# Optimization experiments

Measured on AMD Instinct MI355X. Metric: run time of the kernel, lower is better.

## Reference

```python
import jax, jax.numpy as jnp
import numpy as np

NH = 4
ATT = 16
COL = 64
AIS = 64
B = 8192
SK = 200


def setup_inputs() -> dict:
    key = jax.random.key(0)
    k1, k2, k3, k4, k5 = jax.random.split(key, 5)
    # Xavier-uniform bounds for [fan_in, fan_out] matrices
    def xavier(k, fan_in, fan_out):
        bound = float(np.sqrt(6.0 / (fan_in + fan_out)))
        return jax.random.uniform(k, (fan_in, fan_out), jnp.float32, -bound, bound)
    return {
        "query_input": jax.random.normal(k1, (B, 1, COL), jnp.float32),
        "action_list_input": jax.random.normal(k2, (B, SK, AIS), jnp.float32),
        "Q": xavier(k3, COL, ATT * NH),
        "K": xavier(k4, AIS, ATT * NH),
        "V": xavier(k5, AIS, ATT * NH),
    }


def reference(query_input, action_list_input, Q, K, V):
    b = query_input.shape[0]
    sq = query_input.shape[1]          # == 1 (required by final reshape)
    sk = action_list_input.shape[1]
    # projections
    q = jnp.tensordot(query_input, Q, axes=([-1], [0]))        # [B,Sq,NH*ATT]
    k = jnp.tensordot(action_list_input, K, axes=([-1], [0]))  # [B,Sk,NH*ATT]
    v = jnp.tensordot(action_list_input, V, axes=([-1], [0]))  # [B,Sk,NH*ATT]
    # split heads: chunk along last dim then stack on new leading dim -> [NH,B,S,ATT]
    qh = jnp.transpose(q.reshape(b, sq, NH, ATT), (2, 0, 1, 3))
    kh = jnp.transpose(k.reshape(b, sk, NH, ATT), (2, 0, 1, 3))
    vh = jnp.transpose(v.reshape(b, sk, NH, ATT), (2, 0, 1, 3))
    scores = jnp.einsum("hbqd,hbkd->hbqk", qh, kh) / 8.0       # [NH,B,Sq,Sk]
    attn = jax.nn.softmax(scores, axis=-1)
    res = jnp.einsum("hbqk,hbkd->hbqd", attn, vh)              # [NH,B,Sq,ATT]
    res = jnp.transpose(res, (1, 2, 0, 3))                     # [B,Sq,NH,ATT]
    return res.reshape(b, NH * ATT)
```

## Files before the change

kernel.cpp:

```cpp
#include <hip/hip_runtime.h>

#define NH   4
#define ATT  16
#define COL  64
#define AIS  64
#define SK   200
#define HD   64
#define JP   32
#define AROW 33

typedef _Float16 half2v __attribute__((ext_vector_type(2)));
typedef unsigned int uint32;

static __device__ __forceinline__ half2v u2h(uint32 u) {
    union { uint32 u; half2v h; } x; x.u = u; return x.h;
}

static __device__ __forceinline__ uint32 pk_u32(float a, float b) {
#if __has_builtin(__builtin_amdgcn_cvt_pkrtz)
    union { decltype(__builtin_amdgcn_cvt_pkrtz(0.f, 0.f)) h; uint32 u; } x;
    x.h = __builtin_amdgcn_cvt_pkrtz(a, b);
    return x.u;
#else
    union { half2v h; uint32 u; } x;
    x.h.x = (_Float16)a; x.h.y = (_Float16)b;
    return x.u;
#endif
}

#if __has_builtin(__builtin_amdgcn_fdot2)
#define DOT2(a, b, c) __builtin_amdgcn_fdot2((a), (b), (c), false)
#else
#define DOT2(a, b, c) fmaf((float)(a).x, (float)(b).x, fmaf((float)(a).y, (float)(b).y, (c)))
#endif

__global__ __launch_bounds__(256, 4)
void fused_attn_kernel(const float* __restrict__ query,
                       const float* __restrict__ action,
                       const float* __restrict__ Qw,
                       const float* __restrict__ Kw,
                       const float* __restrict__ Vw,
                       float* __restrict__ out) {
    __shared__ uint32 A2[SK * AROW];
    __shared__ float4 p4_s[SK];
    __shared__ float4 wpart[4][64];
    __shared__ float4 w4_s[64];
    __shared__ float  invd_s[NH];
    __shared__ float  qh_s[HD];
    __shared__ __align__(16) uint32 qk4_s[JP * 4];

    const int b    = blockIdx.x;
    const int t    = threadIdx.x;
    const int lane = t & 63;
    const int wv   = t >> 6;

    const float4* act4 = (const float4*)(action + (size_t)b * (SK * AIS));
    float4 sv[13];
    #pragma unroll
    for (int i = 0; i < 12; ++i) sv[i] = act4[i * 256 + t];
    if (t < 128) sv[12] = act4[3072 + t];

    const float* qb = query + (size_t)b * COL;
    if (t < HD) {
        float acc = 0.f;
        #pragma unroll
        for (int c = 0; c < COL; ++c)
            acc = fmaf(qb[c], Qw[c * HD + t], acc);
        qh_s[t] = acc;
    }
    __syncthreads();

    if (t < 128) {
        const int h = t >> 5, jp = t & 31;
        float a0 = 0.f, a1 = 0.f;
        #pragma unroll
        for (int d = 0; d < ATT; ++d) {
            const float q = qh_s[h * ATT + d];
            a0 = fmaf(q, Kw[(2 * jp)     * HD + h * ATT + d], a0);
            a1 = fmaf(q, Kw[(2 * jp + 1) * HD + h * ATT + d], a1);
        }
        qk4_s[jp * 4 + h] = pk_u32(a0 * 0.125f, a1 * 0.125f);
    }

    #pragma unroll
    for (int i = 0; i < 12; ++i) {
        const int idx = i * 256 + t;
        const float4 v = sv[i];
        const int k   = idx >> 4;
        const int jp0 = (idx & 15) * 2;
        A2[k * AROW + jp0]     = pk_u32(v.x, v.y);
        A2[k * AROW + jp0 + 1] = pk_u32(v.z, v.w);
    }
    if (t < 128) {
        const int idx = 3072 + t;
        const float4 v = sv[12];
        const int k   = idx >> 4;
        const int jp0 = (idx & 15) * 2;
        A2[k * AROW + jp0]     = pk_u32(v.x, v.y);
        A2[k * AROW + jp0 + 1] = pk_u32(v.z, v.w);
    }
    __syncthreads();

    if (t < SK) {
        float a0 = 0.f, a1 = 0.f, a2 = 0.f, a3 = 0.f;
        const int base = t * AROW;
        const uint4* qk4 = (const uint4*)qk4_s;
        #pragma unroll 8
        for (int jp = 0; jp < JP; ++jp) {
            const half2v av = u2h(A2[base + jp]);
            const uint4 q4 = qk4[jp];
            a0 = DOT2(av, u2h(q4.x), a0);
            a1 = DOT2(av, u2h(q4.y), a1);
            a2 = DOT2(av, u2h(q4.z), a2);
            a3 = DOT2(av, u2h(q4.w), a3);
        }
        float4 s; s.x = a0; s.y = a1; s.z = a2; s.w = a3;
        p4_s[t] = s;
    }
    __syncthreads();

    {
        float* pf = (float*)p4_s;
        const int h = wv;
        const float s0 = pf[lane * 4 + h];
        const float s1 = pf[(lane + 64) * 4 + h];
        const float s2 = pf[(lane + 128) * 4 + h];
        const float s3 = (lane < SK - 192) ? pf[(lane + 192) * 4 + h] : -1e30f;
        float m = fmaxf(fmaxf(s0, s1), fmaxf(s2, s3));
        #pragma unroll
        for (int off = 32; off; off >>= 1) m = fmaxf(m, __shfl_xor(m, off));
        const float e0 = __expf(s0 - m);
        const float e1 = __expf(s1 - m);
        const float e2 = __expf(s2 - m);
        const float e3 = (lane < SK - 192) ? __expf(s3 - m) : 0.f;
        pf[lane * 4 + h]         = e0;
        pf[(lane + 64) * 4 + h]  = e1;
        pf[(lane + 128) * 4 + h] = e2;
        if (lane < SK - 192) pf[(lane + 192) * 4 + h] = e3;
        float sum = e0 + e1 + e2 + e3;
        #pragma unroll
        for (int off = 32; off; off >>= 1) sum += __shfl_xor(sum, off);
        if (lane == 0) invd_s[h] = 1.f / sum;
    }
    __syncthreads();

    {
        const int j  = lane;
        const int jp = j >> 1;
        const int k0 = wv * 50;
        float c0 = 0.f, c1 = 0.f, c2 = 0.f, c3 = 0.f;
        #pragma unroll 10
        for (int kk = 0; kk < 50; ++kk) {
            const int k = k0 + kk;
            const float4 p = p4_s[k];
            const half2v av = u2h(A2[k * AROW + jp]);
            const float a = (j & 1) ? (float)av.y : (float)av.x;
            c0 = fmaf(p.x, a, c0);
            c1 = fmaf(p.y, a, c1);
            c2 = fmaf(p.z, a, c2);
            c3 = fmaf(p.w, a, c3);
        }
        float4 c; c.x = c0; c.y = c1; c.z = c2; c.w = c3;
        wpart[wv][j] = c;
    }
    __syncthreads();

    if (t < 64) {
        const float4 r0 = wpart[0][t], r1 = wpart[1][t];
        const float4 r2 = wpart[2][t], r3 = wpart[3][t];
        float4 w;
        w.x = (r0.x + r1.x + r2.x + r3.x) * invd_s[0];
        w.y = (r0.y + r1.y + r2.y + r3.y) * invd_s[1];
        w.z = (r0.z + r1.z + r2.z + r3.z) * invd_s[2];
        w.w = (r0.w + r1.w + r2.w + r3.w) * invd_s[3];
        w4_s[t] = w;
    }
    __syncthreads();

    if (t < 64) {
        const int h = t >> 4;
        const float* wf = (const float*)w4_s;
        float acc = 0.f;
        #pragma unroll
        for (int j = 0; j < AIS; ++j)
            acc = fmaf(wf[j * 4 + h], Vw[j * HD + t], acc);
        out[(size_t)b * HD + t] = acc;
    }
}

extern "C" void kernel_launch(void* const* d_in, const int* in_sizes, int n_in,
                              void* d_out, int out_size, void* d_ws, size_t ws_size,
                              hipStream_t stream) {
    const float* query  = (const float*)d_in[0];
    const float* action = (const float*)d_in[1];
    const float* Qw     = (const float*)d_in[2];
    const float* Kw     = (const float*)d_in[3];
    const float* Vw     = (const float*)d_in[4];
    float* outp = (float*)d_out;

    (void)d_ws; (void)ws_size;

    const int B = in_sizes[0] / COL;
    fused_attn_kernel<<<B, 256, 0, stream>>>(query, action, Qw, Kw, Vw, outp);
}
```

Baseline: 545.3 us.

## Make blocks persistent over 16 batches with double-buffered LDS prefetch

Each workgroup now processes 16 consecutive batch rows instead of one. While the current batch is being computed, it loads the next batch's action tile into registers, then converts and stores it into a second LDS buffer. The Q projection and the q·K products for all 16 batches are computed once up front. This is meant to hide global-load latency behind compute and to spread the setup cost over many rows. The trade-off is a grid of only B/16 workgroups, double the LDS footprint and launch bounds of 2, which lowers occupancy and puts more weight on the in-block barriers.

```diff
diff --git a/kernel.cpp b/kernel.cpp
--- a/kernel.cpp
+++ b/kernel.cpp
@@ -8,6 +8,7 @@
 #define HD   64
 #define JP   32
 #define AROW 33
+#define NBPB 16
 
 typedef _Float16 half2v __attribute__((ext_vector_type(2)));
 typedef unsigned int uint32;
@@ -34,157 +35,202 @@
 #define DOT2(a, b, c) fmaf((float)(a).x, (float)(b).x, fmaf((float)(a).y, (float)(b).y, (c)))
 #endif
 
-__global__ __launch_bounds__(256, 4)
-void fused_attn_kernel(const float* __restrict__ query,
-                       const float* __restrict__ action,
-                       const float* __restrict__ Qw,
-                       const float* __restrict__ Kw,
-                       const float* __restrict__ Vw,
-                       float* __restrict__ out) {
-    __shared__ uint32 A2[SK * AROW];
-    __shared__ float4 p4_s[SK];
-    __shared__ float4 wpart[4][64];
-    __shared__ float4 w4_s[64];
-    __shared__ float  invd_s[NH];
-    __shared__ float  qh_s[HD];
-    __shared__ __align__(16) uint32 qk4_s[JP * 4];
-
-    const int b    = blockIdx.x;
-    const int t    = threadIdx.x;
-    const int lane = t & 63;
-    const int wv   = t >> 6;
-
-    const float4* act4 = (const float4*)(action + (size_t)b * (SK * AIS));
-    float4 sv[13];
-    #pragma unroll
-    for (int i = 0; i < 12; ++i) sv[i] = act4[i * 256 + t];
-    if (t < 128) sv[12] = act4[3072 + t];
-
-    const float* qb = query + (size_t)b * COL;
-    if (t < HD) {
-        float acc = 0.f;
-        #pragma unroll
-        for (int c = 0; c < COL; ++c)
-            acc = fmaf(qb[c], Qw[c * HD + t], acc);
-        qh_s[t] = acc;
-    }
-    __syncthreads();
-
-    if (t < 128) {
-        const int h = t >> 5, jp = t & 31;
-        float a0 = 0.f, a1 = 0.f;
-        #pragma unroll
-        for (int d = 0; d < ATT; ++d) {
-            const float q = qh_s[h * ATT + d];
-            a0 = fmaf(q, Kw[(2 * jp)     * HD + h * ATT + d], a0);
-            a1 = fmaf(q, Kw[(2 * jp + 1) * HD + h * ATT + d], a1);
-        }
-        qk4_s[jp * 4 + h] = pk_u32(a0 * 0.125f, a1 * 0.125f);
-    }
-
-    #pragma unroll
-    for (int i = 0; i < 12; ++i) {
-        const int idx = i * 256 + t;
-        const float4 v = sv[i];
+static __device__ __forceinline__ void wg_barrier() {
+    asm volatile("s_waitcnt lgkmcnt(0)" ::: "memory");
+    __builtin_amdgcn_s_barrier();
+    asm volatile("" ::: "memory");
+}
+
+static __device__ __forceinline__ void issue_loads(float4* sv,
+                                                   const float* __restrict__ action,
+                                                   size_t b, int t) {
+    const float4* a4 = (const float4*)(action + b * (size_t)(SK * AIS));
+    #pragma unroll
+    for (int j = 0; j < 12; ++j) sv[j] = a4[j * 256 + t];
+    if (t < 128) sv[12] = a4[3072 + t];
+}
+
+static __device__ __forceinline__ void convert_store(uint32* __restrict__ dst,
+                                                     const float4* sv, int t) {
+    #pragma unroll
+    for (int j = 0; j < 12; ++j) {
+        const int idx = j * 256 + t;
+        const float4 v = sv[j];
         const int k   = idx >> 4;
         const int jp0 = (idx & 15) * 2;
-        A2[k * AROW + jp0]     = pk_u32(v.x, v.y);
-        A2[k * AROW + jp0 + 1] = pk_u32(v.z, v.w);
+        dst[k * AROW + jp0]     = pk_u32(v.x, v.y);
+        dst[k * AROW + jp0 + 1] = pk_u32(v.z, v.w);
     }
     if (t < 128) {
         const int idx = 3072 + t;
         const float4 v = sv[12];
         const int k   = idx >> 4;
         const int jp0 = (idx & 15) * 2;
-        A2[k * AROW + jp0]     = pk_u32(v.x, v.y);
-        A2[k * AROW + jp0 + 1] = pk_u32(v.z, v.w);
+        dst[k * AROW + jp0]     = pk_u32(v.x, v.y);
+        dst[k * AROW + jp0 + 1] = pk_u32(v.z, v.w);
+    }
+}
+
+__global__ __launch_bounds__(256, 2)
+void fused_attn_persistent(const float* __restrict__ query,
+                           const float* __restrict__ action,
+                           const float* __restrict__ Qw,
+                           const float* __restrict__ Kw,
+                           const float* __restrict__ Vw,
+                           float* __restrict__ out, int nbatch) {
+    __shared__ uint32 A2[2][SK * AROW];
+    __shared__ __align__(16) uint32 qk_all[NBPB * JP * NH];
+    union RunLDS {
+        float qh_all[NBPB][HD];
+        struct { float4 p4[SK]; float4 wpart[4][64]; } r;
+    };
+    __shared__ RunLDS u;
+    __shared__ float invd[NH];
+
+    const int t    = threadIdx.x;
+    const int lane = t & 63;
+    const int wv   = t >> 6;
+    const int b0   = blockIdx.x * NBPB;
+    if (b0 >= nbatch) return;
+
+    float4 sv[13];
+
+    issue_loads(sv, action, (size_t)b0, t);
+
+    #pragma unroll
+    for (int p = 0; p < 4; ++p) {
+        const int bi = p * 4 + wv;
+        const int b  = b0 + bi;
+        float acc = 0.f;
+        if (b < nbatch) {
+            const float4* qb4 = (const float4*)(query + (size_t)b * COL);
+            #pragma unroll
+            for (int c4 = 0; c4 < 16; ++c4) {
+                const float4 qv = qb4[c4];
+                acc = fmaf(qv.x, Qw[(4 * c4 + 0) * HD + lane], acc);
+                acc = fmaf(qv.y, Qw[(4 * c4 + 1) * HD + lane], acc);
+                acc = fmaf(qv.z, Qw[(4 * c4 + 2) * HD + lane], acc);
+                acc = fmaf(qv.w, Qw[(4 * c4 + 3) * HD + lane], acc);
+            }
+        }
+        u.qh_all[bi][lane] = acc;
     }
     __syncthreads();
 
-    if (t < SK) {
-        float a0 = 0.f, a1 = 0.f, a2 = 0.f, a3 = 0.f;
-        const int base = t * AROW;
-        const uint4* qk4 = (const uint4*)qk4_s;
-        #pragma unroll 8
-        for (int jp = 0; jp < JP; ++jp) {
-            const half2v av = u2h(A2[base + jp]);
-            const uint4 q4 = qk4[jp];
-            a0 = DOT2(av, u2h(q4.x), a0);
-            a1 = DOT2(av, u2h(q4.y), a1);
-            a2 = DOT2(av, u2h(q4.z), a2);
-            a3 = DOT2(av, u2h(q4.w), a3);
-        }
-        float4 s; s.x = a0; s.y = a1; s.z = a2; s.w = a3;
-        p4_s[t] = s;
-    }
+    #pragma unroll
+    for (int p = 0; p < 8; ++p) {
+        const int item = p * 256 + t;
+        const int bi   = item >> 7;
+        const int r    = item & 127;
+        const int h    = r >> 5;
+        const int jp   = r & 31;
+        float a0 = 0.f, a1 = 0.f;
+        #pragma unroll
+        for (int d = 0; d < ATT; ++d) {
+            const float q = u.qh_all[bi][h * ATT + d];
+            a0 = fmaf(q, Kw[(2 * jp)     * HD + h * ATT + d], a0);
+            a1 = fmaf(q, Kw[(2 * jp + 1) * HD + h * ATT + d], a1);
+        }
+        qk_all[(bi * JP + jp) * 4 + h] = pk_u32(a0 * 0.125f, a1 * 0.125f);
+    }
+
+    convert_store(&A2[0][0], sv, t);
     __syncthreads();
 
-    {
-        float* pf = (float*)p4_s;
-        const int h = wv;
-        const float s0 = pf[lane * 4 + h];
-        const float s1 = pf[(lane + 64) * 4 + h];
-        const float s2 = pf[(lane + 128) * 4 + h];
-        const float s3 = (lane < SK - 192) ? pf[(lane + 192) * 4 + h] : -1e30f;
-        float m = fmaxf(fmaxf(s0, s1), fmaxf(s2, s3));
-        #pragma unroll
-        for (int off = 32; off; off >>= 1) m = fmaxf(m, __shfl_xor(m, off));
-        const float e0 = __expf(s0 - m);
-        const float e1 = __expf(s1 - m);
-        const float e2 = __expf(s2 - m);
-        const float e3 = (lane < SK - 192) ? __expf(s3 - m) : 0.f;
-        pf[lane * 4 + h]         = e0;
-        pf[(lane + 64) * 4 + h]  = e1;
-        pf[(lane + 128) * 4 + h] = e2;
-        if (lane < SK - 192) pf[(lane + 192) * 4 + h] = e3;
-        float sum = e0 + e1 + e2 + e3;
-        #pragma unroll
-        for (int off = 32; off; off >>= 1) sum += __shfl_xor(sum, off);
-        if (lane == 0) invd_s[h] = 1.f / sum;
-    }
-    __syncthreads();
-
-    {
-        const int j  = lane;
-        const int jp = j >> 1;
-        const int k0 = wv * 50;
-        float c0 = 0.f, c1 = 0.f, c2 = 0.f, c3 = 0.f;
-        #pragma unroll 10
-        for (int kk = 0; kk < 50; ++kk) {
-            const int k = k0 + kk;
-            const float4 p = p4_s[k];
-            const half2v av = u2h(A2[k * AROW + jp]);
-            const float a = (j & 1) ? (float)av.y : (float)av.x;
-            c0 = fmaf(p.x, a, c0);
-            c1 = fmaf(p.y, a, c1);
-            c2 = fmaf(p.z, a, c2);
-            c3 = fmaf(p.w, a, c3);
-        }
-        float4 c; c.x = c0; c.y = c1; c.z = c2; c.w = c3;
-        wpart[wv][j] = c;
-    }
-    __syncthreads();
-
-    if (t < 64) {
-        const float4 r0 = wpart[0][t], r1 = wpart[1][t];
-        const float4 r2 = wpart[2][t], r3 = wpart[3][t];
-        float4 w;
-        w.x = (r0.x + r1.x + r2.x + r3.x) * invd_s[0];
-        w.y = (r0.y + r1.y + r2.y + r3.y) * invd_s[1];
-        w.z = (r0.z + r1.z + r2.z + r3.z) * invd_s[2];
-        w.w = (r0.w + r1.w + r2.w + r3.w) * invd_s[3];
-        w4_s[t] = w;
-    }
-    __syncthreads();
-
-    if (t < 64) {
-        const int h = t >> 4;
-        const float* wf = (const float*)w4_s;
-        float acc = 0.f;
-        #pragma unroll
-        for (int j = 0; j < AIS; ++j)
-            acc = fmaf(wf[j * 4 + h], Vw[j * HD + t], acc);
-        out[(size_t)b * HD + t] = acc;
+    int cur = 0;
+    for (int i = 0; i < NBPB; ++i) {
+        const int  b    = b0 + i;
+        const bool live = (b < nbatch);
+        const bool pre  = (i + 1 < NBPB) && (b + 1 < nbatch);
+
+        if (pre) issue_loads(sv, action, (size_t)(b + 1), t);
+
+        if (live && t < SK) {
+            const uint32* Ab  = &A2[cur][t * AROW];
+            const uint4*  qk4 = (const uint4*)&qk_all[i * JP * 4];
+            float a0 = 0.f, a1 = 0.f, a2 = 0.f, a3 = 0.f;
+            #pragma unroll 8
+            for (int jp = 0; jp < JP; ++jp) {
+                const half2v av = u2h(Ab[jp]);
+                const uint4  q4 = qk4[jp];
+                a0 = DOT2(av, u2h(q4.x), a0);
+                a1 = DOT2(av, u2h(q4.y), a1);
+                a2 = DOT2(av, u2h(q4.z), a2);
+                a3 = DOT2(av, u2h(q4.w), a3);
+            }
+            float4 s; s.x = a0; s.y = a1; s.z = a2; s.w = a3;
+            u.r.p4[t] = s;
+        }
+        wg_barrier();
+
+        if (live) {
+            float* pf = (float*)u.r.p4;
+            const int h = wv;
+            const float s0 = pf[lane * 4 + h];
+            const float s1 = pf[(lane + 64) * 4 + h];
+            const float s2 = pf[(lane + 128) * 4 + h];
+            const float s3 = (lane < SK - 192) ? pf[(lane + 192) * 4 + h] : -1e30f;
+            float m = fmaxf(fmaxf(s0, s1), fmaxf(s2, s3));
+            #pragma unroll
+            for (int off = 32; off; off >>= 1) m = fmaxf(m, __shfl_xor(m, off));
+            const float e0 = __expf(s0 - m);
+            const float e1 = __expf(s1 - m);
+            const float e2 = __expf(s2 - m);
+            const float e3 = (lane < SK - 192) ? __expf(s3 - m) : 0.f;
+            pf[lane * 4 + h]         = e0;
+            pf[(lane + 64) * 4 + h]  = e1;
+            pf[(lane + 128) * 4 + h] = e2;
+            if (lane < SK - 192) pf[(lane + 192) * 4 + h] = e3;
+            float sum = e0 + e1 + e2 + e3;
+            #pragma unroll
+            for (int off = 32; off; off >>= 1) sum += __shfl_xor(sum, off);
+            if (lane == 0) invd[h] = 1.f / sum;
+        }
+        wg_barrier();
+
+        if (live) {
+            const int j  = lane;
+            const int jp = j >> 1;
+            const int k0 = wv * 50;
+            float c0 = 0.f, c1 = 0.f, c2 = 0.f, c3 = 0.f;
+            #pragma unroll 10
+            for (int kk = 0; kk < 50; ++kk) {
+                const int k = k0 + kk;
+                const float4 p  = u.r.p4[k];
+                const half2v av = u2h(A2[cur][k * AROW + jp]);
+                const float a = (j & 1) ? (float)av.y : (float)av.x;
+                c0 = fmaf(p.x, a, c0);
+                c1 = fmaf(p.y, a, c1);
+                c2 = fmaf(p.z, a, c2);
+                c3 = fmaf(p.w, a, c3);
+            }
+            float4 c; c.x = c0; c.y = c1; c.z = c2; c.w = c3;
+            u.r.wpart[wv][j] = c;
+        }
+        wg_barrier();
+
+        if (live && t < 64) {
+            const float4 r0 = u.r.wpart[0][t], r1 = u.r.wpart[1][t];
+            const float4 r2 = u.r.wpart[2][t], r3 = u.r.wpart[3][t];
+            float4 w;
+            w.x = (r0.x + r1.x + r2.x + r3.x) * invd[0];
+            w.y = (r0.y + r1.y + r2.y + r3.y) * invd[1];
+            w.z = (r0.z + r1.z + r2.z + r3.z) * invd[2];
+            w.w = (r0.w + r1.w + r2.w + r3.w) * invd[3];
+            u.r.p4[t] = w;
+            const int h = t >> 4;
+            const float* wf = (const float*)u.r.p4;
+            float acc = 0.f;
+            #pragma unroll
+            for (int j = 0; j < AIS; ++j)
+                acc = fmaf(wf[j * 4 + h], Vw[j * HD + t], acc);
+            out[(size_t)b * HD + t] = acc;
+        }
+
+        if (pre) convert_store(&A2[cur ^ 1][0], sv, t);
+
+        wg_barrier();
+        cur ^= 1;
     }
 }
 
@@ -201,5 +247,7 @@
     (void)d_ws; (void)ws_size;
 
     const int B = in_sizes[0] / COL;
-    fused_attn_kernel<<<B, 256, 0, stream>>>(query, action, Qw, Kw, Vw, outp);
-}
+    const int nblk = (B + NBPB - 1) / NBPB;
+    fused_attn_persistent<<<nblk, 256, 0, stream>>>(query, action, Qw, Kw, Vw,
+                                                    outp, B);
+}
```

New measurement: 660.2 us. 21.1% more time.
